# Performance work log

Hardware: AMD Instinct MI355X
Metric: run time of the kernel (lower is better)

## Reference

```python
import jax, jax.numpy as jnp
import numpy as np

T, H, I, E, SI, TOP_K = 1024, 2048, 1408, 60, 5632, 4


def setup_inputs() -> dict:
    key = jax.random.key(0)
    ks = jax.random.split(key, 9)
    s = 0.02  # typical init scale for weights
    return {
        "x": jax.random.normal(ks[0], (T, H), jnp.float32),
        "router_w": jax.random.normal(ks[1], (E, H), jnp.float32) * s,
        "w_gate": jax.random.normal(ks[2], (E, I, H), jnp.float32) * s,
        "w_up": jax.random.normal(ks[3], (E, I, H), jnp.float32) * s,
        "w_down": jax.random.normal(ks[4], (E, H, I), jnp.float32) * s,
        "sw_gate": jax.random.normal(ks[5], (SI, H), jnp.float32) * s,
        "sw_up": jax.random.normal(ks[6], (SI, H), jnp.float32) * s,
        "sw_down": jax.random.normal(ks[7], (H, SI), jnp.float32) * s,
        "shared_gate_w": jax.random.normal(ks[8], (1, H), jnp.float32) * s,
        "top_k": TOP_K,
    }


def reference(x, router_w, w_gate, w_up, w_down, sw_gate, sw_up, sw_down, shared_gate_w, top_k):
    Ttok, Hdim = x.shape
    Eexp = router_w.shape[0]
    # --- router: softmax over experts, top-k selection (norm_topk_prob=False) ---
    logits = x @ router_w.T                          # [T,E]
    probs = jax.nn.softmax(logits, axis=-1)
    topk_p, topk_i = jax.lax.top_k(probs, top_k)     # [T,k]
    # dense combine weights: zero for unrouted experts
    combine = jnp.zeros((Ttok, Eexp), x.dtype)
    combine = combine.at[jnp.arange(Ttok)[:, None], topk_i].set(topk_p)  # [T,E]

    # --- routed experts: SwiGLU MLP per expert, weighted accumulate (scan over E) ---
    def expert_step(acc, w):
        wg, wu, wd, c = w                            # [I,H],[I,H],[H,I],[T]
        h = jax.nn.silu(x @ wg.T) * (x @ wu.T)       # [T,I]
        return acc + c[:, None] * (h @ wd.T), None

    moe_out, _ = jax.lax.scan(expert_step, jnp.zeros_like(x),
                              (w_gate, w_up, w_down, combine.T))

    # --- shared expert with sigmoid gate ---
    shared = (jax.nn.silu(x @ sw_gate.T) * (x @ sw_up.T)) @ sw_down.T    # [T,H]
    shared = jax.nn.sigmoid(x @ shared_gate_w.T) * shared                # [T,1]*[T,H]
    return moe_out + shared
```

## Files before the change

kernel.cpp:

```cpp
#include <hip/hip_runtime.h>
#include <hip/hip_bf16.h>


typedef float  f32x4  __attribute__((ext_vector_type(4)));
typedef short  bf16x8 __attribute__((ext_vector_type(8)));
typedef unsigned short u16;
typedef unsigned int   u32;

constexpr int TT = 1024, HD = 2048, ID = 1408, NE = 60, SID = 5632, KTOP = 4;
constexpr int NBR_GU = (ID / 128) * NE;
constexpr int NB_GU  = NBR_GU + (SID / 128) * (TT / 128);
constexpr int NBS_DN = (HD / 128) * (TT / 128);
constexpr int NB_DN  = NBS_DN + (HD / 128) * NE;

#define GLDS(g, l) __builtin_amdgcn_global_load_lds( \
    (const __attribute__((address_space(1))) void*)(g), \
    (__attribute__((address_space(3))) void*)(l), 16, 0, 0)
#define GL4(dst, ptr) asm volatile("global_load_dwordx4 %0, %1, off" : "=&v"(dst) : "v"(ptr))
#define WAITVM(n) do { asm volatile("s_waitcnt vmcnt(" #n ")" ::: "memory"); \
                       __builtin_amdgcn_sched_barrier(0); } while (0)
#define BAR() do { asm volatile("" ::: "memory"); \
    __builtin_amdgcn_s_barrier(); \
    asm volatile("" ::: "memory"); } while (0)
#define LGKMBAR() do { asm volatile("s_waitcnt lgkmcnt(0)" ::: "memory"); \
    __builtin_amdgcn_s_barrier(); \
    asm volatile("" ::: "memory"); } while (0)

__device__ __forceinline__ u16 f2bf(float f) {
    union { float f; u32 u; } v; v.f = f;
    u32 r = v.u + 0x7FFFu + ((v.u >> 16) & 1u);
    return (u16)(r >> 16);
}
__device__ __forceinline__ float bf2f(u16 b) {
    union { float f; u32 u; } v; v.u = ((u32)b) << 16; return v.f;
}
__device__ __forceinline__ u32 cvtpk(float a, float b) {
    u32 r; asm("v_cvt_pk_bf16_f32 %0, %1, %2" : "=v"(r) : "v"(a), "v"(b));
    return r;
}
__device__ __forceinline__ bf16x8 cvt8(f32x4 a, f32x4 b) {
    union { u32 u[4]; bf16x8 v; } rr;
    rr.u[0] = cvtpk(a[0], a[1]); rr.u[1] = cvtpk(a[2], a[3]);
    rr.u[2] = cvtpk(b[0], b[1]); rr.u[3] = cvtpk(b[2], b[3]);
    return rr.v;
}
__device__ __forceinline__ int xcd_swz(int bid, int nwg) {
    int q = nwg >> 3, r = nwg & 7;
    int xcd = bid & 7, idx = bid >> 3;
    return (xcd < r ? xcd * (q + 1) : r * (q + 1) + (xcd - r) * q) + idx;
}

__global__ __launch_bounds__(1024) void pscat_k(
    int* __restrict__ cntg, int* __restrict__ basea,
    const float* __restrict__ topk_p, const int* __restrict__ topk_i,
    int* __restrict__ slot_tok, float* __restrict__ slot_wt,
    int* __restrict__ slot_of)
{
    __shared__ int cnt_s[NE];
    __shared__ int base_s[NE];
    __shared__ int fill_s[NE];
    const int t = threadIdx.x;
    if (t < NE) { cnt_s[t] = 0; fill_s[t] = 0; }
    __syncthreads();
    int te[KTOP];
    #pragma unroll
    for (int k = 0; k < KTOP; k++) {
        te[k] = topk_i[t * KTOP + k];
        atomicAdd(&cnt_s[te[k]], 1);
    }
    __syncthreads();
    if (t == 0) {
        int s = 0;
        for (int j = 0; j < NE; j++) { base_s[j] = s; s += cnt_s[j]; }
    }
    __syncthreads();
    if (t < NE) { basea[t] = base_s[t]; cntg[t] = cnt_s[t]; }
    #pragma unroll
    for (int k = 0; k < KTOP; k++) {
        int e = te[k];
        int pos = atomicAdd(&fill_s[e], 1);
        int s = base_s[e] + pos;
        slot_tok[s] = t;
        slot_wt[s]  = topk_p[t * KTOP + k];
        slot_of[t * KTOP + k] = s;
    }
}

__global__ __launch_bounds__(256) void gather_k(
    const u16* __restrict__ dsl, const int* __restrict__ slot_of,
    float* __restrict__ out)
{
    const int t = blockIdx.x;
    const int c = threadIdx.x * 8;
    const int s0 = slot_of[t * 4 + 0], s1 = slot_of[t * 4 + 1];
    const int s2 = slot_of[t * 4 + 2], s3 = slot_of[t * 4 + 3];
    bf16x8 v0 = *(const bf16x8*)&dsl[(size_t)s0 * HD + c];
    bf16x8 v1 = *(const bf16x8*)&dsl[(size_t)s1 * HD + c];
    bf16x8 v2 = *(const bf16x8*)&dsl[(size_t)s2 * HD + c];
    bf16x8 v3 = *(const bf16x8*)&dsl[(size_t)s3 * HD + c];
    float* op = out + (size_t)t * HD + c;
    #pragma unroll
    for (int i = 0; i < 8; i++) {
        float s = bf2f((u16)v0[i]) + bf2f((u16)v1[i])
                + bf2f((u16)v2[i]) + bf2f((u16)v3[i]);
        op[i] += s;
    }
}

__global__ __launch_bounds__(256) void router_k(
    const float* __restrict__ x, const float* __restrict__ rw,
    const float* __restrict__ sgw,
    float* __restrict__ topk_p, int* __restrict__ topk_i,
    float* __restrict__ sgate, u16* __restrict__ xb)
{
    const int wv = threadIdx.x >> 6, l = threadIdx.x & 63;
    const int t = blockIdx.x * 4 + wv;
    const float4* xr = ((const float4*)(x + (size_t)t * HD)) + l * 8;
    float4 xa[8];
    #pragma unroll
    for (int i = 0; i < 8; i++) xa[i] = xr[i];

    {
        u16* xo = xb + (size_t)t * HD + l * 32;
        #pragma unroll
        for (int i = 0; i < 4; i++) {
            uint4 o;
            o.x = cvtpk(xa[2*i].x, xa[2*i].y);
            o.y = cvtpk(xa[2*i].z, xa[2*i].w);
            o.z = cvtpk(xa[2*i+1].x, xa[2*i+1].y);
            o.w = cvtpk(xa[2*i+1].z, xa[2*i+1].w);
            *(uint4*)(xo + i * 8) = o;
        }
    }

    float le = 0.f;
    for (int e = 0; e < NE; e++) {
        const float4* wr = ((const float4*)(rw + (size_t)e * HD)) + l * 8;
        float a = 0.f;
        #pragma unroll
        for (int i = 0; i < 8; i++) {
            float4 wv_ = wr[i];
            a += xa[i].x * wv_.x + xa[i].y * wv_.y + xa[i].z * wv_.z + xa[i].w * wv_.w;
        }
        #pragma unroll
        for (int s = 32; s; s >>= 1) a += __shfl_xor(a, s);
        if (l == e) le = a;
    }
    {
        const float4* wr = ((const float4*)sgw) + l * 8;
        float a = 0.f;
        #pragma unroll
        for (int i = 0; i < 8; i++) {
            float4 wv_ = wr[i];
            a += xa[i].x * wv_.x + xa[i].y * wv_.y + xa[i].z * wv_.z + xa[i].w * wv_.w;
        }
        #pragma unroll
        for (int s = 32; s; s >>= 1) a += __shfl_xor(a, s);
        if (l == 0) sgate[t] = 1.f / (1.f + __expf(-a));
    }
    float mv = (l < NE) ? le : -3.4e38f;
    #pragma unroll
    for (int s = 32; s; s >>= 1) mv = fmaxf(mv, __shfl_xor(mv, s));
    float p = (l < NE) ? __expf(le - mv) : 0.f;
    float ss = p;
    #pragma unroll
    for (int s = 32; s; s >>= 1) ss += __shfl_xor(ss, s);
    p /= ss;
    float pv = (l < NE) ? p : -1.f;
    int   pi = l;
    float kp = 0.f; int ki = 0;
    for (int k = 0; k < KTOP; k++) {
        float bv = pv; int bi = pi;
        #pragma unroll
        for (int s = 32; s; s >>= 1) {
            float ov = __shfl_xor(bv, s); int oi = __shfl_xor(bi, s);
            if (ov > bv || (ov == bv && oi < bi)) { bv = ov; bi = oi; }
        }
        if (l == k) { kp = bv; ki = bi; }
        if (pi == bi) pv = -1.f;
    }
    if (l < KTOP) {
        topk_p[t * KTOP + l] = kp;
        topk_i[t * KTOP + l] = ki;
    }
}

__global__ __launch_bounds__(512, 2) void gu_all(
    const u16* __restrict__ Xb,
    const float* __restrict__ w_gate, const float* __restrict__ w_up,
    const float* __restrict__ sw_g, const float* __restrict__ sw_u,
    u16* __restrict__ h, u16* __restrict__ hs,
    const int* __restrict__ slot_tok, const float* __restrict__ slot_wt,
    const int* __restrict__ cnt, const int* __restrict__ basea)
{
    __shared__ u16 Asl[4][128 * 32];
    __shared__ u16 Bgsl[2][128 * 32];
    __shared__ u16 Busl[2][128 * 32];

    const int lidx = blockIdx.x;
    const int bid = (lidx < NB_GU - NBR_GU) ? (NBR_GU + lidx)
                                            : xcd_swz(lidx - (NB_GU - NBR_GU), NBR_GU);
    const bool grouped = bid < NBR_GU;
    const int tid = threadIdx.x, w = tid >> 6, lane = tid & 63;
    const int lm = lane & 15, lk = lane >> 4;
    const int wm0 = (w >> 2) * 64, wn0 = (w & 3) * 32;

    int e = 0, my = 0, nb;
    const float *Wg, *Wu; u16* Hout; int Nout;
    if (grouped) {
        e = bid / 11; nb = bid % 11;
        Wg = w_gate + (size_t)e * ID * HD; Wu = w_up + (size_t)e * ID * HD;
        Hout = h; Nout = ID;
    } else {
        int sid = bid - NBR_GU; my = sid / 44; nb = sid % 44;
        Wg = sw_g; Wu = sw_u; Hout = hs; Nout = SID;
    }
    const int mcnt  = grouped ? cnt[e] : 128;
    const int mbase = grouped ? basea[e] : 0;

    const int ars = tid >> 2;
    const int aCh = (((tid & 3) ^ (ars & 3) ^ ((ars >> 2) & 3))) << 3;
    const int segA = (w * 16) * 32;
    const int brt = tid >> 2, bkc = tid & 3;
    const float* pg = Wg + (size_t)(nb * 128 + brt) * HD + bkc * 8;
    const float* pu = Wu + (size_t)(nb * 128 + brt) * HD + bkc * 8;
    const int bWr = brt * 32 + ((bkc ^ ((brt >> 1) & 3)) << 3);

    int aOff[4], bOff[2];
    #pragma unroll
    for (int mf = 0; mf < 4; mf++) {
        int r = wm0 + mf * 16 + lm;
        aOff[mf] = r * 32 + ((lk ^ (r & 3) ^ ((r >> 2) & 3)) << 3);
    }
    #pragma unroll
    for (int nf = 0; nf < 2; nf++) {
        int rb = wn0 + nf * 16 + lm;
        bOff[nf] = rb * 32 + ((lk ^ ((rb >> 1) & 3)) << 3);
    }
    const int nk = HD >> 5;

    for (int mt = 0; grouped ? (mt * 128 < mcnt) : (mt == 0); ++mt) {
        const u16* aSrc;
        {
            int row;
            if (grouped) {
                int sl = mbase + mt * 128 + ars;
                row = (mt * 128 + ars < mcnt) ? slot_tok[sl] : slot_tok[mbase];
            } else row = my * 128 + ars;
            aSrc = Xb + (size_t)row * HD + aCh;
        }

        f32x4 accG[4][2], accU[4][2];
        #pragma unroll
        for (int mf = 0; mf < 4; mf++)
            #pragma unroll
            for (int nf = 0; nf < 2; nf++) {
                accG[mf][nf] = f32x4{0.f, 0.f, 0.f, 0.f};
                accU[mf][nf] = f32x4{0.f, 0.f, 0.f, 0.f};
            }

        f32x4 ga0, ga1, ua0, ua1;
        f32x4 gb0, gb1, ub0, ub1;

#define ISSUE(G0_, G1_, U0_, U1_, AB, KT) do {                                \
        GL4(G0_, pg + (KT)); GL4(G1_, pg + (KT) + 4);                         \
        GL4(U0_, pu + (KT)); GL4(U1_, pu + (KT) + 4);                         \
        GLDS(aSrc + (KT), &Asl[AB][segA]);                                    \
    } while (0)

#define WRITEB(G0_, G1_, U0_, U1_, BB) do {                                   \
        *(bf16x8*)&Bgsl[BB][bWr] = cvt8(G0_, G1_);                            \
        *(bf16x8*)&Busl[BB][bWr] = cvt8(U0_, U1_);                            \
    } while (0)

#define COMPSTEP(AB, BB) do {                                                 \
        bf16x8 af[4], bg[2], bu_[2];                                          \
        _Pragma("unroll")                                                     \
        for (int mf = 0; mf < 4; mf++) af[mf] = *(const bf16x8*)&Asl[AB][aOff[mf]]; \
        _Pragma("unroll")                                                     \
        for (int nf = 0; nf < 2; nf++) {                                      \
            bg[nf]  = *(const bf16x8*)&Bgsl[BB][bOff[nf]];                    \
            bu_[nf] = *(const bf16x8*)&Busl[BB][bOff[nf]];                    \
        }                                                                     \
        _Pragma("unroll")                                                     \
        for (int mf = 0; mf < 4; mf++)                                        \
            _Pragma("unroll")                                                 \
            for (int nf = 0; nf < 2; nf++) {                                  \
                accG[mf][nf] = __builtin_amdgcn_mfma_f32_16x16x32_bf16(af[mf], bg[nf],  accG[mf][nf], 0, 0, 0); \
                accU[mf][nf] = __builtin_amdgcn_mfma_f32_16x16x32_bf16(af[mf], bu_[nf], accU[mf][nf], 0, 0, 0); \
            }                                                                 \
    } while (0)

        ISSUE(ga0, ga1, ua0, ua1, 0, 0);
        ISSUE(gb0, gb1, ub0, ub1, 1, 32);
        WAITVM(5);
        WRITEB(ga0, ga1, ua0, ua1, 0);
        LGKMBAR();

        for (int t = 0; t < nk; t += 4) {
            if (t + 2 < nk) { ISSUE(ga0, ga1, ua0, ua1, 2, (t + 2) << 5); COMPSTEP(0, 0); WAITVM(5); }
            else            { COMPSTEP(0, 0); WAITVM(0); }
            if (t + 1 < nk) WRITEB(gb0, gb1, ub0, ub1, 1);
            LGKMBAR();
            if (t + 3 < nk) { ISSUE(gb0, gb1, ub0, ub1, 3, (t + 3) << 5); COMPSTEP(1, 1); WAITVM(5); }
            else            { COMPSTEP(1, 1); WAITVM(0); }
            if (t + 2 < nk) WRITEB(ga0, ga1, ua0, ua1, 0);
            LGKMBAR();
            if (t + 4 < nk) { ISSUE(ga0, ga1, ua0, ua1, 0, (t + 4) << 5); COMPSTEP(2, 0); WAITVM(5); }
            else            { COMPSTEP(2, 0); WAITVM(0); }
            if (t + 3 < nk) WRITEB(gb0, gb1, ub0, ub1, 1);
            LGKMBAR();
            if (t + 5 < nk) { ISSUE(gb0, gb1, ub0, ub1, 1, (t + 5) << 5); COMPSTEP(3, 1); WAITVM(5); }
            else            { COMPSTEP(3, 1); WAITVM(0); }
            if (t + 4 < nk) WRITEB(ga0, ga1, ua0, ua1, 0);
            LGKMBAR();
        }
#undef ISSUE
#undef WRITEB
#undef COMPSTEP

        #pragma unroll
        for (int mf = 0; mf < 4; mf++)
            #pragma unroll
            for (int j = 0; j < 4; j++) {
                int m = wm0 + mf * 16 + lk * 4 + j;
                bool valid = grouped ? (mt * 128 + m < mcnt) : true;
                if (valid) {
                    size_t row; float wt;
                    if (grouped) {
                        size_t sl = (size_t)(mbase + mt * 128 + m);
                        row = sl; wt = slot_wt[sl];
                    } else { row = (size_t)(my * 128 + m); wt = 1.f; }
                    #pragma unroll
                    for (int nf = 0; nf < 2; nf++) {
                        int col = nb * 128 + wn0 + nf * 16 + lm;
                        float g = accG[mf][nf][j], u = accU[mf][nf][j];
                        float hv = g / (1.f + __expf(-g)) * u * wt;
                        Hout[row * (size_t)Nout + col] = f2bf(hv);
                    }
                }
            }
    }
}

__global__ __launch_bounds__(256, 2) void down_all(
    const u16* __restrict__ h, const u16* __restrict__ hs,
    const float* __restrict__ w_down, const float* __restrict__ sw_d,
    float* __restrict__ outF, u16* __restrict__ dsl,
    const float* __restrict__ sgate,
    const int* __restrict__ cnt, const int* __restrict__ basea)
{
    __shared__ u16   Asl[3][128 * 32];
    __shared__ float Bsl[3][128 * 32];

    const int lidx = blockIdx.x;
    const int bid = (lidx < NBS_DN) ? lidx
                                    : (NBS_DN + xcd_swz(lidx - NBS_DN, NB_DN - NBS_DN));
    const bool shared_m = bid < NBS_DN;
    const int tid = threadIdx.x, w = tid >> 6, lane = tid & 63;
    const int lm = lane & 15, lk = lane >> 4;
    const int wm0 = (w >> 1) * 64, wn0 = (w & 1) * 64;

    int e = 0, my = 0, nb, K;
    const u16* Ap; const float* Wp;
    if (shared_m) {
        my = bid / 16; nb = bid % 16; K = SID; Ap = hs; Wp = sw_d;
    } else {
        int rid = bid - NBS_DN; e = rid / 16; nb = rid % 16; K = ID;
        Ap = h; Wp = w_down + (size_t)e * HD * ID;
    }
    const int mcnt  = shared_m ? 128 : cnt[e];
    const int mbase = shared_m ? 0 : basea[e];

    const int aCh = (((lane & 3) ^ ((lane >> 2) & 3) ^ ((lane >> 4) & 3))) << 3;
    const int bCh = ((lane & 7) ^ ((lane >> 3) & 7)) << 2;

    const float* bSrc[4];
    #pragma unroll
    for (int j = 0; j < 4; j++) {
        size_t rB = (size_t)(nb * 128 + w * 32 + j * 8 + (lane >> 3));
        bSrc[j] = Wp + rB * K + bCh;
    }

    int aOff[4], bOff[4][2];
    #pragma unroll
    for (int mf = 0; mf < 4; mf++) {
        int r = wm0 + mf * 16 + lm;
        aOff[mf] = r * 32 + ((lk ^ (r & 3) ^ ((r >> 2) & 3)) << 3);
    }
    #pragma unroll
    for (int nf = 0; nf < 4; nf++) {
        int rb = wn0 + nf * 16 + lm;
        bOff[nf][0] = rb * 32 + ((((lk << 1)    ) ^ (rb & 7)) << 2);
        bOff[nf][1] = rb * 32 + ((((lk << 1) | 1) ^ (rb & 7)) << 2);
    }

    const int nk = K >> 5;

    for (int mt = 0; shared_m ? (mt == 0) : (mt * 128 < mcnt); ++mt) {
        const u16* aSrc[2];
        #pragma unroll
        for (int j = 0; j < 2; j++) {
            int mrow = w * 32 + j * 16 + (lane >> 2);
            size_t row = shared_m ? (size_t)(my * 128 + mrow)
                                  : (size_t)(mbase + mt * 128 + mrow);
            aSrc[j] = Ap + row * K + aCh;
        }

        f32x4 acc[4][4];
        #pragma unroll
        for (int mf = 0; mf < 4; mf++)
            #pragma unroll
            for (int nf = 0; nf < 4; nf++) acc[mf][nf] = f32x4{0.f, 0.f, 0.f, 0.f};

        auto stage = [&](int b, int kt) {
            #pragma unroll
            for (int j = 0; j < 2; j++)
                GLDS(aSrc[j] + kt, &Asl[b][(w * 32 + j * 16) * 32]);
            #pragma unroll
            for (int j = 0; j < 4; j++)
                GLDS(bSrc[j] + kt, &Bsl[b][(w * 32 + j * 8) * 32]);
        };
        auto comp = [&](int b) {
            const u16*   At = Asl[b];
            const float* Bt = Bsl[b];
            bf16x8 af[4];
            #pragma unroll
            for (int mf = 0; mf < 4; mf++) af[mf] = *(const bf16x8*)&At[aOff[mf]];
            #pragma unroll
            for (int nf = 0; nf < 4; nf++) {
                bf16x8 bf_ = cvt8(*(const f32x4*)&Bt[bOff[nf][0]],
                                  *(const f32x4*)&Bt[bOff[nf][1]]);
                #pragma unroll
                for (int mf = 0; mf < 4; mf++)
                    acc[mf][nf] = __builtin_amdgcn_mfma_f32_16x16x32_bf16(af[mf], bf_, acc[mf][nf], 0, 0, 0);
            }
        };

        stage(0, 0); stage(1, 32);
        int t = 0, cb = 0;
        for (; t + 2 < nk; ++t) {
            int sbuf = cb - 1; if (sbuf < 0) sbuf += 3;
            stage(sbuf, (t + 2) << 5);
            WAITVM(12); BAR(); comp(cb); BAR();
            cb = (cb + 1 == 3) ? 0 : cb + 1;
        }
        WAITVM(6); BAR(); comp(cb); BAR();
        cb = (cb + 1 == 3) ? 0 : cb + 1;
        WAITVM(0); BAR(); comp(cb); BAR();

        #pragma unroll
        for (int mf = 0; mf < 4; mf++)
            #pragma unroll
            for (int j = 0; j < 4; j++) {
                int m = wm0 + mf * 16 + lk * 4 + j;
                if (mt * 128 + m < mcnt) {
                    if (shared_m) {
                        int tok = my * 128 + m;
                        float sc = sgate[tok];
                        #pragma unroll
                        for (int nf = 0; nf < 4; nf++) {
                            int col = nb * 128 + wn0 + nf * 16 + lm;
                            outF[(size_t)tok * HD + col] = sc * acc[mf][nf][j];
                        }
                    } else {
                        size_t srow = (size_t)(mbase + mt * 128 + m);
                        #pragma unroll
                        for (int nf = 0; nf < 4; nf++) {
                            int col = nb * 128 + wn0 + nf * 16 + lm;
                            dsl[srow * HD + col] = f2bf(acc[mf][nf][j]);
                        }
                    }
                }
            }
    }
}

extern "C" void kernel_launch(void* const* d_in, const int* in_sizes, int n_in,
                              void* d_out, int out_size, void* d_ws, size_t ws_size,
                              hipStream_t stream)
{
    const float* x      = (const float*)d_in[0];
    const float* rw     = (const float*)d_in[1];
    const float* w_gate = (const float*)d_in[2];
    const float* w_up   = (const float*)d_in[3];
    const float* w_down = (const float*)d_in[4];
    const float* sw_g   = (const float*)d_in[5];
    const float* sw_u   = (const float*)d_in[6];
    const float* sw_d   = (const float*)d_in[7];
    const float* sgw    = (const float*)d_in[8];
    float* out = (float*)d_out;

    char* ws = (char*)d_ws;
    int*   cnt      = (int*)(ws + 0);
    int*   basea    = (int*)(ws + 512);
    float* sgate    = (float*)(ws + 768);
    float* topk_p   = (float*)(ws + 5120);
    int*   topk_i   = (int*)(ws + 21504);
    int*   slot_tok = (int*)(ws + 37888);
    float* slot_wt  = (float*)(ws + 54272);
    u16*   xb = (u16*)(ws + 71680);
    u16*   h  = xb + (size_t)TT * HD;
    u16*   hs = h + (size_t)(4096 + 128) * ID;
    u16*   dsl = hs + (size_t)TT * SID;
    int*   slot_of = (int*)(dsl + (size_t)(4096 + 128) * HD);

    router_k<<<TT / 4, 256, 0, stream>>>(x, rw, sgw, topk_p, topk_i, sgate, xb);
    pscat_k<<<1, 1024, 0, stream>>>(cnt, basea, topk_p, topk_i,
                                    slot_tok, slot_wt, slot_of);

    gu_all<<<NB_GU, 512, 0, stream>>>(
        xb, w_gate, w_up, sw_g, sw_u, h, hs,
        slot_tok, slot_wt, cnt, basea);

    down_all<<<NB_DN, 256, 0, stream>>>(
        h, hs, w_down, sw_d, out, dsl,
        sgate, cnt, basea);

    gather_k<<<TT, 256, 0, stream>>>(dsl, slot_of, out);
}
```

Measured before the change: 684.4 us.

## Use 256-row M tiles for shared-expert gate/up GEMM to halve weight conversion traffic

Shared-expert gate/up blocks now cover 256 token rows instead of 128, reusing each converted fp32->bf16 weight tile across two A sub-tiles. This halves the number of shared blocks and the repeated reading and converting of sw_gate/sw_up weights. In exchange it doubles accumulator registers, drops the two-blocks-per-CU launch bound, and doubles A LDS buffers, which can reduce occupancy, including for the routed-expert path that shares the kernel.

Result: slower. 804.7 us (+17.6%).

```diff
diff --git a/kernel.cpp b/kernel.cpp
--- a/kernel.cpp
+++ b/kernel.cpp
@@ -9,7 +9,8 @@
 
 constexpr int TT = 1024, HD = 2048, ID = 1408, NE = 60, SID = 5632, KTOP = 4;
 constexpr int NBR_GU = (ID / 128) * NE;
-constexpr int NB_GU  = NBR_GU + (SID / 128) * (TT / 128);
+constexpr int NBS_GU = (SID / 128) * (TT / 256);
+constexpr int NB_GU  = NBR_GU + NBS_GU;
 constexpr int NBS_DN = (HD / 128) * (TT / 128);
 constexpr int NB_DN  = NBS_DN + (HD / 128) * NE;
 
@@ -185,7 +186,7 @@
     }
 }
 
-__global__ __launch_bounds__(512, 2) void gu_all(
+__global__ __launch_bounds__(512) void gu_all(
     const u16* __restrict__ Xb,
     const float* __restrict__ w_gate, const float* __restrict__ w_up,
     const float* __restrict__ sw_g, const float* __restrict__ sw_u,
@@ -193,34 +194,32 @@
     const int* __restrict__ slot_tok, const float* __restrict__ slot_wt,
     const int* __restrict__ cnt, const int* __restrict__ basea)
 {
-    __shared__ u16 Asl[4][128 * 32];
+    __shared__ u16 Asl[4][256 * 32];
     __shared__ u16 Bgsl[2][128 * 32];
     __shared__ u16 Busl[2][128 * 32];
 
     const int lidx = blockIdx.x;
-    const int bid = (lidx < NB_GU - NBR_GU) ? (NBR_GU + lidx)
-                                            : xcd_swz(lidx - (NB_GU - NBR_GU), NBR_GU);
+    const int bid = (lidx < NBS_GU) ? (NBR_GU + lidx)
+                                    : xcd_swz(lidx - NBS_GU, NBR_GU);
     const bool grouped = bid < NBR_GU;
     const int tid = threadIdx.x, w = tid >> 6, lane = tid & 63;
     const int lm = lane & 15, lk = lane >> 4;
     const int wm0 = (w >> 2) * 64, wn0 = (w & 3) * 32;
 
     int e = 0, my = 0, nb;
-    const float *Wg, *Wu; u16* Hout; int Nout;
+    const float *Wg, *Wu;
     if (grouped) {
         e = bid / 11; nb = bid % 11;
         Wg = w_gate + (size_t)e * ID * HD; Wu = w_up + (size_t)e * ID * HD;
-        Hout = h; Nout = ID;
     } else {
         int sid = bid - NBR_GU; my = sid / 44; nb = sid % 44;
-        Wg = sw_g; Wu = sw_u; Hout = hs; Nout = SID;
-    }
-    const int mcnt  = grouped ? cnt[e] : 128;
-    const int mbase = grouped ? basea[e] : 0;
+        Wg = sw_g; Wu = sw_u;
+    }
 
     const int ars = tid >> 2;
     const int aCh = (((tid & 3) ^ (ars & 3) ^ ((ars >> 2) & 3))) << 3;
-    const int segA = (w * 16) * 32;
+    const int segA  = (w * 16) * 32;
+    const int segA2 = (128 + w * 16) * 32;
     const int brt = tid >> 2, bkc = tid & 3;
     const float* pg = Wg + (size_t)(nb * 128 + brt) * HD + bkc * 8;
     const float* pu = Wu + (size_t)(nb * 128 + brt) * HD + bkc * 8;
@@ -239,28 +238,28 @@
     }
     const int nk = HD >> 5;
 
-    for (int mt = 0; grouped ? (mt * 128 < mcnt) : (mt == 0); ++mt) {
-        const u16* aSrc;
-        {
-            int row;
-            if (grouped) {
+    if (grouped) {
+        const int mcnt  = cnt[e];
+        const int mbase = basea[e];
+        for (int mt = 0; mt * 128 < mcnt; ++mt) {
+            const u16* aSrc;
+            {
                 int sl = mbase + mt * 128 + ars;
-                row = (mt * 128 + ars < mcnt) ? slot_tok[sl] : slot_tok[mbase];
-            } else row = my * 128 + ars;
-            aSrc = Xb + (size_t)row * HD + aCh;
-        }
-
-        f32x4 accG[4][2], accU[4][2];
-        #pragma unroll
-        for (int mf = 0; mf < 4; mf++)
-            #pragma unroll
-            for (int nf = 0; nf < 2; nf++) {
-                accG[mf][nf] = f32x4{0.f, 0.f, 0.f, 0.f};
-                accU[mf][nf] = f32x4{0.f, 0.f, 0.f, 0.f};
+                int row = (mt * 128 + ars < mcnt) ? slot_tok[sl] : slot_tok[mbase];
+                aSrc = Xb + (size_t)row * HD + aCh;
             }
 
-        f32x4 ga0, ga1, ua0, ua1;
-        f32x4 gb0, gb1, ub0, ub1;
+            f32x4 accG[4][2], accU[4][2];
+            #pragma unroll
+            for (int mf = 0; mf < 4; mf++)
+                #pragma unroll
+                for (int nf = 0; nf < 2; nf++) {
+                    accG[mf][nf] = f32x4{0.f, 0.f, 0.f, 0.f};
+                    accU[mf][nf] = f32x4{0.f, 0.f, 0.f, 0.f};
+                }
+
+            f32x4 ga0, ga1, ua0, ua1;
+            f32x4 gb0, gb1, ub0, ub1;
 
 #define ISSUE(G0_, G1_, U0_, U1_, AB, KT) do {                                \
         GL4(G0_, pg + (KT)); GL4(G1_, pg + (KT) + 4);                         \
@@ -291,53 +290,152 @@
             }                                                                 \
     } while (0)
 
-        ISSUE(ga0, ga1, ua0, ua1, 0, 0);
-        ISSUE(gb0, gb1, ub0, ub1, 1, 32);
-        WAITVM(5);
-        WRITEB(ga0, ga1, ua0, ua1, 0);
-        LGKMBAR();
-
-        for (int t = 0; t < nk; t += 4) {
-            if (t + 2 < nk) { ISSUE(ga0, ga1, ua0, ua1, 2, (t + 2) << 5); COMPSTEP(0, 0); WAITVM(5); }
-            else            { COMPSTEP(0, 0); WAITVM(0); }
-            if (t + 1 < nk) WRITEB(gb0, gb1, ub0, ub1, 1);
+            ISSUE(ga0, ga1, ua0, ua1, 0, 0);
+            ISSUE(gb0, gb1, ub0, ub1, 1, 32);
+            WAITVM(5);
+            WRITEB(ga0, ga1, ua0, ua1, 0);
             LGKMBAR();
-            if (t + 3 < nk) { ISSUE(gb0, gb1, ub0, ub1, 3, (t + 3) << 5); COMPSTEP(1, 1); WAITVM(5); }
-            else            { COMPSTEP(1, 1); WAITVM(0); }
-            if (t + 2 < nk) WRITEB(ga0, ga1, ua0, ua1, 0);
-            LGKMBAR();
-            if (t + 4 < nk) { ISSUE(ga0, ga1, ua0, ua1, 0, (t + 4) << 5); COMPSTEP(2, 0); WAITVM(5); }
-            else            { COMPSTEP(2, 0); WAITVM(0); }
-            if (t + 3 < nk) WRITEB(gb0, gb1, ub0, ub1, 1);
-            LGKMBAR();
-            if (t + 5 < nk) { ISSUE(gb0, gb1, ub0, ub1, 1, (t + 5) << 5); COMPSTEP(3, 1); WAITVM(5); }
-            else            { COMPSTEP(3, 1); WAITVM(0); }
-            if (t + 4 < nk) WRITEB(ga0, ga1, ua0, ua1, 0);
-            LGKMBAR();
-        }
+
+            for (int t = 0; t < nk; t += 4) {
+                if (t + 2 < nk) { ISSUE(ga0, ga1, ua0, ua1, 2, (t + 2) << 5); COMPSTEP(0, 0); WAITVM(5); }
+                else            { COMPSTEP(0, 0); WAITVM(0); }
+                if (t + 1 < nk) WRITEB(gb0, gb1, ub0, ub1, 1);
+                LGKMBAR();
+                if (t + 3 < nk) { ISSUE(gb0, gb1, ub0, ub1, 3, (t + 3) << 5); COMPSTEP(1, 1); WAITVM(5); }
+                else            { COMPSTEP(1, 1); WAITVM(0); }
+                if (t + 2 < nk) WRITEB(ga0, ga1, ua0, ua1, 0);
+                LGKMBAR();
+                if (t + 4 < nk) { ISSUE(ga0, ga1, ua0, ua1, 0, (t + 4) << 5); COMPSTEP(2, 0); WAITVM(5); }
+                else            { COMPSTEP(2, 0); WAITVM(0); }
+                if (t + 3 < nk) WRITEB(gb0, gb1, ub0, ub1, 1);
+                LGKMBAR();
+                if (t + 5 < nk) { ISSUE(gb0, gb1, ub0, ub1, 1, (t + 5) << 5); COMPSTEP(3, 1); WAITVM(5); }
+                else            { COMPSTEP(3, 1); WAITVM(0); }
+                if (t + 4 < nk) WRITEB(ga0, ga1, ua0, ua1, 0);
+                LGKMBAR();
+            }
 #undef ISSUE
 #undef WRITEB
 #undef COMPSTEP
 
+            #pragma unroll
+            for (int mf = 0; mf < 4; mf++)
+                #pragma unroll
+                for (int j = 0; j < 4; j++) {
+                    int m = wm0 + mf * 16 + lk * 4 + j;
+                    if (mt * 128 + m < mcnt) {
+                        size_t sl = (size_t)(mbase + mt * 128 + m);
+                        float wt = slot_wt[sl];
+                        #pragma unroll
+                        for (int nf = 0; nf < 2; nf++) {
+                            int col = nb * 128 + wn0 + nf * 16 + lm;
+                            float g = accG[mf][nf][j], u = accU[mf][nf][j];
+                            float hv = g / (1.f + __expf(-g)) * u * wt;
+                            h[sl * (size_t)ID + col] = f2bf(hv);
+                        }
+                    }
+                }
+        }
+    } else {
+        const u16* aSrc1 = Xb + (size_t)(my * 256 + ars) * HD + aCh;
+        const u16* aSrc2 = aSrc1 + (size_t)128 * HD;
+
+        f32x4 acG[4][2], acU[4][2];
+        f32x4 acG2[4][2], acU2[4][2];
+        #pragma unroll
+        for (int mf = 0; mf < 4; mf++)
+            #pragma unroll
+            for (int nf = 0; nf < 2; nf++) {
+                acG[mf][nf]  = f32x4{0.f, 0.f, 0.f, 0.f};
+                acU[mf][nf]  = f32x4{0.f, 0.f, 0.f, 0.f};
+                acG2[mf][nf] = f32x4{0.f, 0.f, 0.f, 0.f};
+                acU2[mf][nf] = f32x4{0.f, 0.f, 0.f, 0.f};
+            }
+
+        f32x4 ga0, ga1, ua0, ua1;
+        f32x4 gb0, gb1, ub0, ub1;
+
+#define ISSUE2(G0_, G1_, U0_, U1_, AB, KT) do {                               \
+        GL4(G0_, pg + (KT)); GL4(G1_, pg + (KT) + 4);                         \
+        GL4(U0_, pu + (KT)); GL4(U1_, pu + (KT) + 4);                         \
+        GLDS(aSrc1 + (KT), &Asl[AB][segA]);                                   \
+        GLDS(aSrc2 + (KT), &Asl[AB][segA2]);                                  \
+    } while (0)
+
+#define WRITEB2(G0_, G1_, U0_, U1_, BB) do {                                  \
+        *(bf16x8*)&Bgsl[BB][bWr] = cvt8(G0_, G1_);                            \
+        *(bf16x8*)&Busl[BB][bWr] = cvt8(U0_, U1_);                            \
+    } while (0)
+
+#define COMPSTEP2(AB, BB) do {                                                \
+        bf16x8 bg[2], bu_[2];                                                 \
+        _Pragma("unroll")                                                     \
+        for (int nf = 0; nf < 2; nf++) {                                      \
+            bg[nf]  = *(const bf16x8*)&Bgsl[BB][bOff[nf]];                    \
+            bu_[nf] = *(const bf16x8*)&Busl[BB][bOff[nf]];                    \
+        }                                                                     \
+        _Pragma("unroll")                                                     \
+        for (int mf = 0; mf < 4; mf++) {                                      \
+            bf16x8 af = *(const bf16x8*)&Asl[AB][aOff[mf]];                   \
+            _Pragma("unroll")                                                 \
+            for (int nf = 0; nf < 2; nf++) {                                  \
+                acG[mf][nf] = __builtin_amdgcn_mfma_f32_16x16x32_bf16(af, bg[nf],  acG[mf][nf], 0, 0, 0); \
+                acU[mf][nf] = __builtin_amdgcn_mfma_f32_16x16x32_bf16(af, bu_[nf], acU[mf][nf], 0, 0, 0); \
+            }                                                                 \
+        }                                                                     \
+        _Pragma("unroll")                                                     \
+        for (int mf = 0; mf < 4; mf++) {                                      \
+            bf16x8 af = *(const bf16x8*)&Asl[AB][aOff[mf] + 128 * 32];        \
+            _Pragma("unroll")                                                 \
+            for (int nf = 0; nf < 2; nf++) {                                  \
+                acG2[mf][nf] = __builtin_amdgcn_mfma_f32_16x16x32_bf16(af, bg[nf],  acG2[mf][nf], 0, 0, 0); \
+                acU2[mf][nf] = __builtin_amdgcn_mfma_f32_16x16x32_bf16(af, bu_[nf], acU2[mf][nf], 0, 0, 0); \
+            }                                                                 \
+        }                                                                     \
+    } while (0)
+
+        ISSUE2(ga0, ga1, ua0, ua1, 0, 0);
+        ISSUE2(gb0, gb1, ub0, ub1, 1, 32);
+        WAITVM(6);
+        WRITEB2(ga0, ga1, ua0, ua1, 0);
+        LGKMBAR();
+
+        for (int t = 0; t < nk; t += 4) {
+            if (t + 2 < nk) { ISSUE2(ga0, ga1, ua0, ua1, 2, (t + 2) << 5); COMPSTEP2(0, 0); WAITVM(6); }
+            else            { COMPSTEP2(0, 0); WAITVM(0); }
+            if (t + 1 < nk) WRITEB2(gb0, gb1, ub0, ub1, 1);
+            LGKMBAR();
+            if (t + 3 < nk) { ISSUE2(gb0, gb1, ub0, ub1, 3, (t + 3) << 5); COMPSTEP2(1, 1); WAITVM(6); }
+            else            { COMPSTEP2(1, 1); WAITVM(0); }
+            if (t + 2 < nk) WRITEB2(ga0, ga1, ua0, ua1, 0);
+            LGKMBAR();
+            if (t + 4 < nk) { ISSUE2(ga0, ga1, ua0, ua1, 0, (t + 4) << 5); COMPSTEP2(2, 0); WAITVM(6); }
+            else            { COMPSTEP2(2, 0); WAITVM(0); }
+            if (t + 3 < nk) WRITEB2(gb0, gb1, ub0, ub1, 1);
+            LGKMBAR();
+            if (t + 5 < nk) { ISSUE2(gb0, gb1, ub0, ub1, 1, (t + 5) << 5); COMPSTEP2(3, 1); WAITVM(6); }
+            else            { COMPSTEP2(3, 1); WAITVM(0); }
+            if (t + 4 < nk) WRITEB2(ga0, ga1, ua0, ua1, 0);
+            LGKMBAR();
+        }
+#undef ISSUE2
+#undef WRITEB2
+#undef COMPSTEP2
+
         #pragma unroll
         for (int mf = 0; mf < 4; mf++)
             #pragma unroll
             for (int j = 0; j < 4; j++) {
                 int m = wm0 + mf * 16 + lk * 4 + j;
-                bool valid = grouped ? (mt * 128 + m < mcnt) : true;
-                if (valid) {
-                    size_t row; float wt;
-                    if (grouped) {
-                        size_t sl = (size_t)(mbase + mt * 128 + m);
-                        row = sl; wt = slot_wt[sl];
-                    } else { row = (size_t)(my * 128 + m); wt = 1.f; }
-                    #pragma unroll
-                    for (int nf = 0; nf < 2; nf++) {
-                        int col = nb * 128 + wn0 + nf * 16 + lm;
-                        float g = accG[mf][nf][j], u = accU[mf][nf][j];
-                        float hv = g / (1.f + __expf(-g)) * u * wt;
-                        Hout[row * (size_t)Nout + col] = f2bf(hv);
-                    }
+                size_t row1 = (size_t)(my * 256 + m);
+                size_t row2 = row1 + 128;
+                #pragma unroll
+                for (int nf = 0; nf < 2; nf++) {
+                    int col = nb * 128 + wn0 + nf * 16 + lm;
+                    float g1 = acG[mf][nf][j], u1 = acU[mf][nf][j];
+                    hs[row1 * (size_t)SID + col] = f2bf(g1 / (1.f + __expf(-g1)) * u1);
+                    float g2 = acG2[mf][nf][j], u2 = acU2[mf][nf][j];
+                    hs[row2 * (size_t)SID + col] = f2bf(g2 / (1.f + __expf(-g2)) * u2);
                 }
             }
     }
```
